# Kernel optimization log

Hardware: AMD Instinct MI355X
Metric: run time of the kernel (lower is better)

## Reference

```python
import jax, jax.numpy as jnp
import numpy as np

# Model dims (DeepSeek/LLaMA-class, GQA)
B, S = 1, 2048          # one prefill sequence -> total tokens T = B*S
H, KVH, D = 32, 8, 128  # query heads, kv heads, head_size
HID = H * D             # hidden_size = 4096
T = B * S
NUM_SLOTS = 4096        # paged KV-cache slots
ROPE_THETA = 10000.0


def _apply_rope(x, cos, sin):
    # x: [T, heads, D]; cos/sin: [T, D//2] (NeoX rotate-halves style)
    d2 = x.shape[-1] // 2
    x1, x2 = x[..., :d2], x[..., d2:]
    c = cos[:, None, :]
    s = sin[:, None, :]
    return jnp.concatenate([x1 * c - x2 * s, x2 * c + x1 * s], axis=-1)


def setup_inputs() -> dict:
    key = jax.random.key(0)
    k1, k2, k3 = jax.random.split(key, 3)
    hidden_states = jax.random.normal(k1, (T, HID), dtype=jnp.float32)
    w_qkv = jax.random.normal(k2, (HID, H * D + 2 * KVH * D), dtype=jnp.float32) * 0.02
    w_o = jax.random.normal(k3, (H * D, HID), dtype=jnp.float32) * 0.02
    # rotary tables from true positions (prefill: positions 0..S-1 per sequence)
    positions = jnp.tile(jnp.arange(S, dtype=jnp.float32), B)  # [T]
    inv_freq = 1.0 / (ROPE_THETA ** (jnp.arange(0, D, 2, dtype=jnp.float32) / D))  # [D//2]
    freqs = positions[:, None] * inv_freq[None, :]  # [T, D//2]
    cos, sin = jnp.cos(freqs), jnp.sin(freqs)
    k_cache = jnp.zeros((NUM_SLOTS, KVH, D), dtype=jnp.float32)
    v_cache = jnp.zeros((NUM_SLOTS, KVH, D), dtype=jnp.float32)
    slots = jnp.arange(T, dtype=jnp.int32)  # one slot per new token
    return {"hidden_states": hidden_states, "cos": cos, "sin": sin,
            "w_qkv": w_qkv, "w_o": w_o,
            "k_cache": k_cache, "v_cache": v_cache, "slots": slots}


def reference(hidden_states, cos, sin, w_qkv, w_o, k_cache, v_cache, slots):
    scale = D ** -0.5
    # fused QKV projection, split like torch .split([H*D, 2*KVH*D], dim=1)
    qkv = hidden_states @ w_qkv                      # [T, H*D + 2*KVH*D]
    q = qkv[:, :H * D].reshape(T, H, D)
    kv = qkv[:, H * D:].reshape(T, 2, KVH, D)
    k, v = kv[:, 0], kv[:, 1]
    # RoPE applied to query and key (not value)
    q = _apply_rope(q, cos, sin)
    k = _apply_rope(k, cos, sin)
    # reshape_and_cache: scatter post-RoPE K / raw V into the paged cache slots
    k_cache_new = k_cache.at[slots].set(k)
    v_cache_new = v_cache.at[slots].set(v)
    # prefill varlen attention with equal-length sequences -> dense causal GQA
    qb = q.reshape(B, S, H, D)
    groups = H // KVH
    kb = jnp.repeat(k.reshape(B, S, KVH, D), groups, axis=2)  # [B,S,H,D]
    vb = jnp.repeat(v.reshape(B, S, KVH, D), groups, axis=2)
    scores = jnp.einsum("bqhd,bkhd->bhqk", qb, kb) * scale    # [B,H,S,S]
    causal = jnp.tril(jnp.ones((S, S), dtype=bool))
    scores = jnp.where(causal[None, None], scores, jnp.finfo(scores.dtype).min)
    probs = jax.nn.softmax(scores, axis=-1)
    attn = jnp.einsum("bhqk,bkhd->bqhd", probs, vb)           # [B,S,H,D]
    out = attn.reshape(T, H * D) @ w_o                        # o_proj
    return out, k_cache_new, v_cache_new
```

## Files before the change

### kernel.cpp

```cpp
#include <hip/hip_runtime.h>
#include <stdint.h>
#include <stddef.h>
#include <type_traits>

#define TK      2048
#define HIDDEN  4096
#define NHEAD   32
#define NKV     8
#define DH      128
#define NQKVC   6144
#define NSLOTS  4096
#define GROUPS  4

typedef __attribute__((ext_vector_type(8))) short  short8;
typedef __attribute__((ext_vector_type(4))) short  short4v;
typedef __attribute__((ext_vector_type(4))) float  float4v;

__device__ __forceinline__ unsigned short f2bf(float f) {
  union { float f; unsigned u; } v; v.f = f;
  return (unsigned short)((v.u + 0x7FFFu + ((v.u >> 16) & 1u)) >> 16);
}
__device__ __forceinline__ float bf2f(unsigned short b) {
  union { unsigned u; float f; } v; v.u = ((unsigned)b) << 16;
  return v.f;
}

__device__ __forceinline__ void gload_lds16(const unsigned short* g, unsigned short* l) {
  __builtin_amdgcn_global_load_lds(
      (const __attribute__((address_space(1))) void*)g,
      (__attribute__((address_space(3))) void*)l, 16, 0, 0);
}

__global__ __launch_bounds__(256) void convert_f32_bf16(
    const float* __restrict__ src, unsigned short* __restrict__ dst, int n4) {
  int i = blockIdx.x * blockDim.x + threadIdx.x;
  int stride = gridDim.x * blockDim.x;
  for (; i < n4; i += stride) {
    float4v v = *(const float4v*)(src + (size_t)i * 4);
    short4v o;
#pragma unroll
    for (int j = 0; j < 4; ++j) o[j] = (short)f2bf(v[j]);
    *(short4v*)(dst + (size_t)i * 4) = o;
  }
}

__global__ __launch_bounds__(256) void transpose_convert(
    const float* __restrict__ src, unsigned short* __restrict__ dst,
    int K, int N) {
  __shared__ float tile[64][65];
  int k0 = blockIdx.y * 64, n0 = blockIdx.x * 64;
  int tc = threadIdx.x & 63, tr = threadIdx.x >> 6;
#pragma unroll
  for (int i = 0; i < 16; ++i) {
    int r = tr + 4 * i;
    tile[r][tc] = src[(size_t)(k0 + r) * N + n0 + tc];
  }
  __syncthreads();
#pragma unroll
  for (int i = 0; i < 16; ++i) {
    int r = tr + 4 * i;
    dst[(size_t)(n0 + r) * K + k0 + tc] = f2bf(tile[tc][r]);
  }
}

__global__ __launch_bounds__(256) void v_transpose(
    const unsigned short* __restrict__ qkv, unsigned short* __restrict__ vt) {
  __shared__ unsigned short tile[64][72];
  int t0 = blockIdx.x * 64, e0 = blockIdx.y * 64;
  int tid = threadIdx.x;
  int lrow = tid >> 4, lcol = (tid & 15) * 4;
#pragma unroll
  for (int i = 0; i < 4; ++i) {
    int r = i * 16 + lrow;
    *(short4v*)&tile[r][lcol] =
        *(const short4v*)&qkv[(size_t)(t0 + r) * NQKVC + 5120 + e0 + lcol];
  }
  __syncthreads();
  int tc = tid & 63, tr = tid >> 6;
#pragma unroll
  for (int i = 0; i < 16; ++i) {
    int e = tr + 4 * i;
    vt[(size_t)(e0 + e) * TK + t0 + tc] = tile[tc][e];
  }
}

template <typename OutT>
__global__ __launch_bounds__(256) void gemm_bt(
    const unsigned short* __restrict__ A,
    const unsigned short* __restrict__ BT,
    OutT* __restrict__ C,
    int M, int N, int K) {
  __shared__ unsigned short As[128][64];
  __shared__ unsigned short Bs[128][64];
  int m0 = blockIdx.y * 128, n0 = blockIdx.x * 128;
  int tid = threadIdx.x;
  int lane = tid & 63, w = tid >> 6;
  int wr = (w >> 1) * 64, wc = (w & 1) * 64;
  int lr = lane & 15, lg = lane >> 4;
  int srow = lane >> 3;
  int scol = ((lane & 7) ^ (srow & 7)) * 8;

  float4v acc[4][4] = {};

  for (int k0 = 0; k0 < K; k0 += 64) {
#pragma unroll
    for (int i = 0; i < 4; ++i) {
      int row = w * 32 + i * 8;
      gload_lds16(A + (size_t)(m0 + row + srow) * K + k0 + scol, &As[row][0]);
      gload_lds16(BT + (size_t)(n0 + row + srow) * K + k0 + scol, &Bs[row][0]);
    }
    __syncthreads();
#pragma unroll
    for (int kk = 0; kk < 64; kk += 32) {
      int cc = (((kk >> 3) + lg) ^ (lr & 7)) * 8;
      short8 a[4], b[4];
#pragma unroll
      for (int mi = 0; mi < 4; ++mi) a[mi] = *(const short8*)&As[wr + mi * 16 + lr][cc];
#pragma unroll
      for (int ni = 0; ni < 4; ++ni) b[ni] = *(const short8*)&Bs[wc + ni * 16 + lr][cc];
#pragma unroll
      for (int mi = 0; mi < 4; ++mi)
#pragma unroll
        for (int ni = 0; ni < 4; ++ni)
          acc[mi][ni] = __builtin_amdgcn_mfma_f32_16x16x32_bf16(a[mi], b[ni], acc[mi][ni], 0, 0, 0);
    }
    __syncthreads();
  }

  int orow = (lane >> 4) * 4;
#pragma unroll
  for (int mi = 0; mi < 4; ++mi)
#pragma unroll
    for (int ni = 0; ni < 4; ++ni)
#pragma unroll
      for (int r = 0; r < 4; ++r) {
        float v = acc[mi][ni][r];
        size_t idx = (size_t)(m0 + wr + mi * 16 + orow + r) * N + n0 + wc + ni * 16 + lr;
        if constexpr (std::is_same<OutT, unsigned short>::value)
          C[idx] = f2bf(v);
        else
          C[idx] = v;
      }
}

__global__ __launch_bounds__(256) void rope_scatter(
    const unsigned short* __restrict__ qkv,
    const float* __restrict__ cosb,
    const float* __restrict__ sinb,
    const int* __restrict__ slots,
    unsigned short* __restrict__ qout,
    unsigned short* __restrict__ kout,
    float* __restrict__ kcache,
    float* __restrict__ vcache) {
  int t = blockIdx.x;
  int tid = threadIdx.x;
  int slot = slots[t];
  const unsigned short* row = qkv + (size_t)t * NQKVC;

#pragma unroll
  for (int i = 0; i < 8; ++i) {
    int p = tid + 256 * i;
    int h = p >> 6, d = p & 63;
    float x1 = bf2f(row[h * 128 + d]);
    float x2 = bf2f(row[h * 128 + d + 64]);
    float c = cosb[t * 64 + d], s = sinb[t * 64 + d];
    qout[(size_t)t * HIDDEN + h * 128 + d]      = f2bf(x1 * c - x2 * s);
    qout[(size_t)t * HIDDEN + h * 128 + d + 64] = f2bf(x2 * c + x1 * s);
  }
#pragma unroll
  for (int i = 0; i < 2; ++i) {
    int p = tid + 256 * i;
    int kh = p >> 6, d = p & 63;
    float x1 = bf2f(row[4096 + kh * 128 + d]);
    float x2 = bf2f(row[4096 + kh * 128 + d + 64]);
    float c = cosb[t * 64 + d], s = sinb[t * 64 + d];
    float o1 = x1 * c - x2 * s, o2 = x2 * c + x1 * s;
    kout[t * 1024 + kh * 128 + d]      = f2bf(o1);
    kout[t * 1024 + kh * 128 + d + 64] = f2bf(o2);
    kcache[(size_t)slot * 1024 + kh * 128 + d]      = o1;
    kcache[(size_t)slot * 1024 + kh * 128 + d + 64] = o2;
  }
#pragma unroll
  for (int i = 0; i < 4; ++i) {
    int e = tid + 256 * i;
    vcache[(size_t)slot * 1024 + e] = bf2f(row[5120 + e]);
  }
}

__global__ __launch_bounds__(256) void attn_kernel(
    const unsigned short* __restrict__ q,
    const unsigned short* __restrict__ k,
    const unsigned short* __restrict__ vt,
    unsigned short* __restrict__ attn) {
  __shared__ unsigned short Ks[2][32][128];
  __shared__ unsigned short Vs[2][128][32];
  __shared__ unsigned short Ps[4][16][40];

  const int h = blockIdx.y;
  const int g = h >> 2;
  const int tid = threadIdx.x, lane = tid & 63, w = tid >> 6;
  const int lr = lane & 15, lg = lane >> 4;
  const float scale = 0.08838834764831845f;

  const int ksrow = lane >> 4;
  const int vsrow = lane >> 2;
  const int vscc = ((lane & 3) ^ (vsrow & 3)) * 8;

  for (int half = 0; half < 2; ++half) {
    const int q0 = (half == 0 ? (31 - (int)blockIdx.x) : (int)blockIdx.x) * 64;
    const int nt = (q0 >> 5) + 2;

    short8 qf[4];
    int qrow = q0 + w * 16 + lr;
#pragma unroll
    for (int c = 0; c < 4; ++c)
      qf[c] = *(const short8*)(q + (size_t)qrow * HIDDEN + h * DH + c * 32 + lg * 8);

    float4v accO[8] = {};
    float m[4], l[4];
#pragma unroll
    for (int r = 0; r < 4; ++r) { m[r] = -1e30f; l[r] = 0.f; }

#pragma unroll
    for (int i = 0; i < 2; ++i) {
      int krow = w * 8 + i * 4;
      int kcc = ((lane & 15) ^ ((krow + ksrow) & 7)) * 8;
      gload_lds16(k + ((size_t)(krow + ksrow) * NKV + g) * DH + kcc, &Ks[0][krow][0]);
      int vrow = w * 32 + i * 16;
      gload_lds16(vt + (size_t)(g * DH + vrow + vsrow) * TK + vscc, &Vs[0][vrow][0]);
    }

    int cur = 0;
    for (int it = 0; it < nt; ++it) {
      int kv0 = it << 5;
      __syncthreads();
      if (it + 1 < nt) {
        int kv1 = kv0 + 32;
#pragma unroll
        for (int i = 0; i < 2; ++i) {
          int krow = w * 8 + i * 4;
          int kcc = ((lane & 15) ^ ((krow + ksrow) & 7)) * 8;
          gload_lds16(k + ((size_t)(kv1 + krow + ksrow) * NKV + g) * DH + kcc,
                      &Ks[cur ^ 1][krow][0]);
          int vrow = w * 32 + i * 16;
          gload_lds16(vt + (size_t)(g * DH + vrow + vsrow) * TK + kv1 + vscc,
                      &Vs[cur ^ 1][vrow][0]);
        }
      }

      float4v s0 = {}, s1 = {};
#pragma unroll
      for (int c = 0; c < 4; ++c) {
        int cc = ((c * 4 + lg) ^ (lr & 7)) * 8;
        short8 b0 = *(const short8*)&Ks[cur][lr][cc];
        short8 b1 = *(const short8*)&Ks[cur][16 + lr][cc];
        s0 = __builtin_amdgcn_mfma_f32_16x16x32_bf16(qf[c], b0, s0, 0, 0, 0);
        s1 = __builtin_amdgcn_mfma_f32_16x16x32_bf16(qf[c], b1, s1, 0, 0, 0);
      }

      int qg = q0 + w * 16 + lg * 4;
      bool domask = (kv0 + 31 > q0 + w * 16);
      float p0[4], p1[4], fac[4];
#pragma unroll
      for (int r = 0; r < 4; ++r) {
        float v0 = s0[r] * scale, v1 = s1[r] * scale;
        if (domask) {
          if (kv0 + lr > qg + r)      v0 = -1e30f;
          if (kv0 + 16 + lr > qg + r) v1 = -1e30f;
        }
        float mt = fmaxf(v0, v1);
#pragma unroll
        for (int msk = 8; msk >= 1; msk >>= 1) mt = fmaxf(mt, __shfl_xor(mt, msk));
        float mn = fmaxf(m[r], mt);
        float f = __expf(m[r] - mn);
        p0[r] = __expf(v0 - mn);
        p1[r] = __expf(v1 - mn);
        float rs = p0[r] + p1[r];
#pragma unroll
        for (int msk = 8; msk >= 1; msk >>= 1) rs += __shfl_xor(rs, msk);
        l[r] = l[r] * f + rs;
        m[r] = mn;
        fac[r] = f;
      }
#pragma unroll
      for (int ni = 0; ni < 8; ++ni)
#pragma unroll
        for (int r = 0; r < 4; ++r) accO[ni][r] *= fac[r];

#pragma unroll
      for (int r = 0; r < 4; ++r) {
        Ps[w][lg * 4 + r][lr]      = f2bf(p0[r]);
        Ps[w][lg * 4 + r][16 + lr] = f2bf(p1[r]);
      }
      short8 pa = *(const short8*)&Ps[w][lr][lg * 8];
      int vcc = (lg ^ (lr & 3)) * 8;
#pragma unroll
      for (int ni = 0; ni < 8; ++ni) {
        short8 bv = *(const short8*)&Vs[cur][ni * 16 + lr][vcc];
        accO[ni] = __builtin_amdgcn_mfma_f32_16x16x32_bf16(pa, bv, accO[ni], 0, 0, 0);
      }
      cur ^= 1;
    }
    __syncthreads();

#pragma unroll
    for (int ni = 0; ni < 8; ++ni)
#pragma unroll
      for (int r = 0; r < 4; ++r) {
        int row = q0 + w * 16 + lg * 4 + r;
        attn[(size_t)row * HIDDEN + h * DH + ni * 16 + lr] = f2bf(accO[ni][r] / l[r]);
      }
  }
}

extern "C" void kernel_launch(void* const* d_in, const int* in_sizes, int n_in,
                              void* d_out, int out_size, void* d_ws, size_t ws_size,
                              hipStream_t stream) {
  const float* hidden  = (const float*)d_in[0];
  const float* cosb    = (const float*)d_in[1];
  const float* sinb    = (const float*)d_in[2];
  const float* w_qkv   = (const float*)d_in[3];
  const float* w_o     = (const float*)d_in[4];
  const float* k_cache = (const float*)d_in[5];
  const float* v_cache = (const float*)d_in[6];
  const int*   slots   = (const int*)d_in[7];

  float* out = (float*)d_out;
  float* kco = out + (size_t)TK * HIDDEN;
  float* vco = kco + (size_t)NSLOTS * NKV * DH;

  char* ws = (char*)d_ws;
  const size_t MB = 1024 * 1024;
  unsigned short* hid_bf = (unsigned short*)(ws + 0);
  unsigned short* wqkvT  = (unsigned short*)(ws + 16 * MB);
  unsigned short* woT    = (unsigned short*)(ws + 64 * MB);
  unsigned short* qkvb   = (unsigned short*)(ws + 96 * MB);
  unsigned short* qb     = (unsigned short*)(ws + 120 * MB);
  unsigned short* kb     = (unsigned short*)(ws + 136 * MB);
  unsigned short* vtb    = (unsigned short*)(ws + 140 * MB);
  unsigned short* attnb  = hid_bf;

  convert_f32_bf16<<<2048, 256, 0, stream>>>(hidden, hid_bf, TK * HIDDEN / 4);
  transpose_convert<<<dim3(NQKVC / 64, HIDDEN / 64), 256, 0, stream>>>(
      w_qkv, wqkvT, HIDDEN, NQKVC);
  transpose_convert<<<dim3(HIDDEN / 64, HIDDEN / 64), 256, 0, stream>>>(
      w_o, woT, HIDDEN, HIDDEN);

  gemm_bt<unsigned short><<<dim3(NQKVC / 128, TK / 128), 256, 0, stream>>>(
      hid_bf, wqkvT, qkvb, TK, NQKVC, HIDDEN);

  hipMemcpyAsync(kco, k_cache, (size_t)NSLOTS * NKV * DH * 4,
                 hipMemcpyDeviceToDevice, stream);
  hipMemcpyAsync(vco, v_cache, (size_t)NSLOTS * NKV * DH * 4,
                 hipMemcpyDeviceToDevice, stream);

  rope_scatter<<<TK, 256, 0, stream>>>(qkvb, cosb, sinb, slots,
                                       qb, kb, kco, vco);
  v_transpose<<<dim3(TK / 64, 16), 256, 0, stream>>>(qkvb, vtb);

  attn_kernel<<<dim3(16, NHEAD), 256, 0, stream>>>(qb, kb, vtb, attnb);

  gemm_bt<float><<<dim3(HIDDEN / 128, TK / 128), 256, 0, stream>>>(
      attnb, woT, out, TK, HIDDEN, HIDDEN);
}
```

Baseline: 616.7 us.

## Widen attention KV tile to 64, fold scale into Q, lazy rescale

The attention kernel now processes 64 keys per iteration instead of 32, which halves the loop trip count and the barrier and softmax overhead per key. The softmax scale and log2(e) are folded into Q during RoPE so the kernel can use exp2f without a per-score multiply. Rescaling of the running max and accumulator is skipped unless the max grows by more than 8, and s_setprio is wrapped around the MFMA sections. The cost is double the LDS for K, V and P, and some extra wasted work on the causal diagonal tile.

```diff
diff --git a/kernel.cpp b/kernel.cpp
--- a/kernel.cpp
+++ b/kernel.cpp
@@ -152,6 +152,7 @@
     unsigned short* __restrict__ kout,
     float* __restrict__ kcache,
     float* __restrict__ vcache) {
+  const float SC2 = 0.08838834764831845f * 1.4426950408889634f;
   int t = blockIdx.x;
   int tid = threadIdx.x;
   int slot = slots[t];
@@ -164,8 +165,8 @@
     float x1 = bf2f(row[h * 128 + d]);
     float x2 = bf2f(row[h * 128 + d + 64]);
     float c = cosb[t * 64 + d], s = sinb[t * 64 + d];
-    qout[(size_t)t * HIDDEN + h * 128 + d]      = f2bf(x1 * c - x2 * s);
-    qout[(size_t)t * HIDDEN + h * 128 + d + 64] = f2bf(x2 * c + x1 * s);
+    qout[(size_t)t * HIDDEN + h * 128 + d]      = f2bf((x1 * c - x2 * s) * SC2);
+    qout[(size_t)t * HIDDEN + h * 128 + d + 64] = f2bf((x2 * c + x1 * s) * SC2);
   }
 #pragma unroll
   for (int i = 0; i < 2; ++i) {
@@ -192,23 +193,22 @@
     const unsigned short* __restrict__ k,
     const unsigned short* __restrict__ vt,
     unsigned short* __restrict__ attn) {
-  __shared__ unsigned short Ks[2][32][128];
-  __shared__ unsigned short Vs[2][128][32];
-  __shared__ unsigned short Ps[4][16][40];
+  __shared__ unsigned short Ks[2][64][128];
+  __shared__ unsigned short Vs[2][128][64];
+  __shared__ unsigned short Ps[4][16][72];
 
   const int h = blockIdx.y;
   const int g = h >> 2;
   const int tid = threadIdx.x, lane = tid & 63, w = tid >> 6;
   const int lr = lane & 15, lg = lane >> 4;
-  const float scale = 0.08838834764831845f;
 
   const int ksrow = lane >> 4;
-  const int vsrow = lane >> 2;
-  const int vscc = ((lane & 3) ^ (vsrow & 3)) * 8;
+  const int vsrow = lane >> 3;
+  const int vscc  = ((lane & 7) ^ (vsrow & 7)) * 8;
 
   for (int half = 0; half < 2; ++half) {
     const int q0 = (half == 0 ? (31 - (int)blockIdx.x) : (int)blockIdx.x) * 64;
-    const int nt = (q0 >> 5) + 2;
+    const int nt = (q0 >> 6) + 1;
 
     short8 qf[4];
     int qrow = q0 + w * 16 + lr;
@@ -222,83 +222,92 @@
     for (int r = 0; r < 4; ++r) { m[r] = -1e30f; l[r] = 0.f; }
 
 #pragma unroll
-    for (int i = 0; i < 2; ++i) {
-      int krow = w * 8 + i * 4;
+    for (int i = 0; i < 4; ++i) {
+      int krow = w * 16 + i * 4;
       int kcc = ((lane & 15) ^ ((krow + ksrow) & 7)) * 8;
       gload_lds16(k + ((size_t)(krow + ksrow) * NKV + g) * DH + kcc, &Ks[0][krow][0]);
-      int vrow = w * 32 + i * 16;
+      int vrow = w * 32 + i * 8;
       gload_lds16(vt + (size_t)(g * DH + vrow + vsrow) * TK + vscc, &Vs[0][vrow][0]);
     }
 
     int cur = 0;
     for (int it = 0; it < nt; ++it) {
-      int kv0 = it << 5;
+      int kv0 = it << 6;
       __syncthreads();
       if (it + 1 < nt) {
-        int kv1 = kv0 + 32;
-#pragma unroll
-        for (int i = 0; i < 2; ++i) {
-          int krow = w * 8 + i * 4;
+        int kv1 = kv0 + 64;
+#pragma unroll
+        for (int i = 0; i < 4; ++i) {
+          int krow = w * 16 + i * 4;
           int kcc = ((lane & 15) ^ ((krow + ksrow) & 7)) * 8;
           gload_lds16(k + ((size_t)(kv1 + krow + ksrow) * NKV + g) * DH + kcc,
                       &Ks[cur ^ 1][krow][0]);
-          int vrow = w * 32 + i * 16;
+          int vrow = w * 32 + i * 8;
           gload_lds16(vt + (size_t)(g * DH + vrow + vsrow) * TK + kv1 + vscc,
                       &Vs[cur ^ 1][vrow][0]);
         }
       }
 
-      float4v s0 = {}, s1 = {};
+      float4v s[4] = {};
+      __builtin_amdgcn_s_setprio(1);
 #pragma unroll
       for (int c = 0; c < 4; ++c) {
         int cc = ((c * 4 + lg) ^ (lr & 7)) * 8;
-        short8 b0 = *(const short8*)&Ks[cur][lr][cc];
-        short8 b1 = *(const short8*)&Ks[cur][16 + lr][cc];
-        s0 = __builtin_amdgcn_mfma_f32_16x16x32_bf16(qf[c], b0, s0, 0, 0, 0);
-        s1 = __builtin_amdgcn_mfma_f32_16x16x32_bf16(qf[c], b1, s1, 0, 0, 0);
-      }
+#pragma unroll
+        for (int jt = 0; jt < 4; ++jt) {
+          short8 b = *(const short8*)&Ks[cur][jt * 16 + lr][cc];
+          s[jt] = __builtin_amdgcn_mfma_f32_16x16x32_bf16(qf[c], b, s[jt], 0, 0, 0);
+        }
+      }
+      __builtin_amdgcn_s_setprio(0);
 
       int qg = q0 + w * 16 + lg * 4;
-      bool domask = (kv0 + 31 > q0 + w * 16);
-      float p0[4], p1[4], fac[4];
+      bool domask = (kv0 + 63 > q0 + w * 16);
 #pragma unroll
       for (int r = 0; r < 4; ++r) {
-        float v0 = s0[r] * scale, v1 = s1[r] * scale;
+        float v0 = s[0][r], v1 = s[1][r], v2 = s[2][r], v3 = s[3][r];
         if (domask) {
-          if (kv0 + lr > qg + r)      v0 = -1e30f;
+          if (kv0 + lr      > qg + r) v0 = -1e30f;
           if (kv0 + 16 + lr > qg + r) v1 = -1e30f;
+          if (kv0 + 32 + lr > qg + r) v2 = -1e30f;
+          if (kv0 + 48 + lr > qg + r) v3 = -1e30f;
         }
-        float mt = fmaxf(v0, v1);
+        float mt = fmaxf(fmaxf(v0, v1), fmaxf(v2, v3));
 #pragma unroll
         for (int msk = 8; msk >= 1; msk >>= 1) mt = fmaxf(mt, __shfl_xor(mt, msk));
-        float mn = fmaxf(m[r], mt);
-        float f = __expf(m[r] - mn);
-        p0[r] = __expf(v0 - mn);
-        p1[r] = __expf(v1 - mn);
-        float rs = p0[r] + p1[r];
+        if (__any(mt > m[r] + 8.f)) {
+          float mn = fmaxf(m[r], mt);
+          float f = exp2f(m[r] - mn);
+          m[r] = mn;
+          l[r] *= f;
+#pragma unroll
+          for (int ni = 0; ni < 8; ++ni) accO[ni][r] *= f;
+        }
+        float p0 = exp2f(v0 - m[r]), p1 = exp2f(v1 - m[r]);
+        float p2 = exp2f(v2 - m[r]), p3 = exp2f(v3 - m[r]);
+        float rs = (p0 + p1) + (p2 + p3);
 #pragma unroll
         for (int msk = 8; msk >= 1; msk >>= 1) rs += __shfl_xor(rs, msk);
-        l[r] = l[r] * f + rs;
-        m[r] = mn;
-        fac[r] = f;
-      }
-#pragma unroll
-      for (int ni = 0; ni < 8; ++ni)
-#pragma unroll
-        for (int r = 0; r < 4; ++r) accO[ni][r] *= fac[r];
-
-#pragma unroll
-      for (int r = 0; r < 4; ++r) {
-        Ps[w][lg * 4 + r][lr]      = f2bf(p0[r]);
-        Ps[w][lg * 4 + r][16 + lr] = f2bf(p1[r]);
-      }
-      short8 pa = *(const short8*)&Ps[w][lr][lg * 8];
-      int vcc = (lg ^ (lr & 3)) * 8;
+        l[r] += rs;
+        Ps[w][lg * 4 + r][lr]      = f2bf(p0);
+        Ps[w][lg * 4 + r][16 + lr] = f2bf(p1);
+        Ps[w][lg * 4 + r][32 + lr] = f2bf(p2);
+        Ps[w][lg * 4 + r][48 + lr] = f2bf(p3);
+      }
+
+      short8 pa0 = *(const short8*)&Ps[w][lr][lg * 8];
+      short8 pa1 = *(const short8*)&Ps[w][lr][32 + lg * 8];
+      int cc0 = ((0 * 4 + lg) ^ (lr & 7)) * 8;
+      int cc1 = ((1 * 4 + lg) ^ (lr & 7)) * 8;
+      __builtin_amdgcn_s_setprio(1);
 #pragma unroll
       for (int ni = 0; ni < 8; ++ni) {
-        short8 bv = *(const short8*)&Vs[cur][ni * 16 + lr][vcc];
-        accO[ni] = __builtin_amdgcn_mfma_f32_16x16x32_bf16(pa, bv, accO[ni], 0, 0, 0);
-      }
+        short8 bv0 = *(const short8*)&Vs[cur][ni * 16 + lr][cc0];
+        short8 bv1 = *(const short8*)&Vs[cur][ni * 16 + lr][cc1];
+        accO[ni] = __builtin_amdgcn_mfma_f32_16x16x32_bf16(pa0, bv0, accO[ni], 0, 0, 0);
+        accO[ni] = __builtin_amdgcn_mfma_f32_16x16x32_bf16(pa1, bv1, accO[ni], 0, 0, 0);
+      }
+      __builtin_amdgcn_s_setprio(0);
       cur ^= 1;
     }
     __syncthreads();
```

Result: faster. 603.2 us (-2.2%).
